# Optimization experiments

Measured on AMD Instinct MI355X. Metric: run time of the kernel, lower is better.

The kernel has to match this reference:

```python
import jax, jax.numpy as jnp
import numpy as np

B, T, C, H = 2, 2048, 2048, 16
HD = C // H  # 128
WINDOW = 2048


def setup_inputs() -> dict:
    key = jax.random.key(0)
    k0, k1, k2 = jax.random.split(key, 3)
    s = 0.02  # GPT-2 style init scale
    return {
        "x": jax.random.normal(k0, (B, T, C), jnp.float32),
        "w_attn": jax.random.normal(k1, (3 * C, C), jnp.float32) * s,
        "b_attn": jnp.zeros((3 * C,), jnp.float32),
        "w_proj": jax.random.normal(k2, (C, C), jnp.float32) * s,
        "b_proj": jnp.zeros((C,), jnp.float32),
    }


def reference(x, w_attn, b_attn, w_proj, b_proj):
    Bb, Tt, Cc = x.shape
    # fused qkv projection (torch Linear: y = x @ W^T + b)
    qkv = x @ w_attn.T + b_attn                       # [B, T, 3C]
    q, k, v = jnp.split(qkv, 3, axis=2)

    def to_heads(t):
        return t.reshape(Bb, Tt, H, HD).transpose(0, 2, 1, 3)  # [B, H, T, HD]

    q, k, v = to_heads(q), to_heads(k), to_heads(v)
    K = k.shape[2]  # kv length (== T, no past_kv)

    attn = jnp.einsum('bhqd,bhkd->bhqk', q, k) / jnp.sqrt(jnp.float32(HD))
    # Faithful to source: mask[:, :, T-1:T, :K] — single tril row T-1 broadcast
    # over all query positions (for prefill K==T this row is all ones).
    mask_row = jnp.arange(K) <= (Tt - 1)              # [K] bool
    attn = jnp.where(mask_row[None, None, None, :], attn, -jnp.inf)
    weights = jax.nn.softmax(attn, axis=-1)            # [B, H, T, K]
    # dropout p=0.0 (eval): identity
    ctx = jnp.einsum('bhqk,bhkd->bhqd', weights, v)    # [B, H, T, HD]
    ctx = ctx.transpose(0, 2, 1, 3).reshape(Bb, Tt, Cc)
    out = ctx @ w_proj.T + b_proj                      # [B, T, C]
    return (out, k, v)  # (context, present_kv)
```

## Files before the change

### kernel.cpp

```cpp
#include <hip/hip_runtime.h>
#include <hip/hip_bf16.h>
#include <cstdint>
#include <cstddef>
#include <cmath>

typedef __attribute__((ext_vector_type(8))) short short8;
typedef __attribute__((ext_vector_type(4))) short bf16x4;
typedef __attribute__((ext_vector_type(4))) float f32x4;

static constexpr int BB = 2, T = 2048, C = 2048, H = 16, HD = 128;
static constexpr int M = BB * T;
static constexpr size_t BTC = (size_t)BB * T * C;

__device__ __forceinline__ short f2bf(float f) {
    union { float f; uint32_t u; } v; v.f = f;
    uint32_t u = v.u;
    uint32_t r = (u + 0x7fffu + ((u >> 16) & 1u)) >> 16;
    return (short)r;
}

__device__ __forceinline__ short f2bf_fast(float f) {
    __hip_bfloat16 h = __float2bfloat16(f);
    return *reinterpret_cast<short*>(&h);
}

__device__ __forceinline__ void gl_lds16(const void* g, void* l) {
    __builtin_amdgcn_global_load_lds(
        (const __attribute__((address_space(1))) unsigned int*)g,
        (__attribute__((address_space(3))) unsigned int*)l, 16, 0, 0);
}

__global__ void cvt_bf16(const float* __restrict__ in, short* __restrict__ out, int n) {
    int i = (blockIdx.x * 256 + threadIdx.x) * 8;
    if (i >= n) return;
    float4 a = *(const float4*)(in + i);
    float4 b = *(const float4*)(in + i + 4);
    short8 o;
    o[0] = f2bf(a.x); o[1] = f2bf(a.y); o[2] = f2bf(a.z); o[3] = f2bf(a.w);
    o[4] = f2bf(b.x); o[5] = f2bf(b.y); o[6] = f2bf(b.z); o[7] = f2bf(b.w);
    *(short8*)(out + i) = o;
}

__launch_bounds__(512, 2)
__global__ void gemm_qkv256(const short* __restrict__ A, const short* __restrict__ Bw,
                            const float* __restrict__ bias, float* __restrict__ outF,
                            short* __restrict__ q_ws, short* __restrict__ k_ws) {
    extern __shared__ char lds[];
    constexpr int K = 2048, NKT = K / 64;
    constexpr int BUFSZ = 57344;

    int bid = blockIdx.x;
    int swz = (bid & 7) * 64 + (bid >> 3);
    int by = swz >> 5, bx = swz & 31;
    int row0 = by * 256, col0 = bx * 192;

    int t = threadIdx.x, w = t >> 6, l = t & 63;
    int lr = l & 15, lg = l >> 4;
    int wr = w >> 2, wc = w & 3;

    const char* Ab = (const char*)A;
    const char* Bb = (const char*)Bw;
    const char* srcb[7];
    int dstoff[7];
#pragma unroll
    for (int c = 0; c < 7; c++) {
        bool isA = c < 4;
        int coff = (isA ? c : c - 4) * 8192 + t * 16;
        int row = coff >> 7;
        int colb = (coff & 127) ^ ((row & 7) << 4);
        srcb[c] = isA ? Ab + (size_t)(row0 + row) * (K * 2) + colb
                      : Bb + (size_t)(col0 + row) * (K * 2) + colb;
        dstoff[c] = (isA ? 0 : 32768) + coff;
    }

    f32x4 acc[8][3] = {};

#pragma unroll
    for (int c = 0; c < 7; c++) gl_lds16(srcb[c], lds + dstoff[c]);
#pragma unroll
    for (int c = 0; c < 7; c++) gl_lds16(srcb[c] + 128, lds + BUFSZ + dstoff[c]);
    asm volatile("s_waitcnt vmcnt(7)" ::: "memory");
    __builtin_amdgcn_s_barrier();

    for (int kt = 0; kt < NKT; kt++) {
        const char* Abase = lds + (kt & 1) * BUFSZ;
        const char* Bbase = Abase + 32768;

        short8 bfr[3][2];
#pragma unroll
        for (int p = 0; p < 4; p++) {
            short8 af[2][2];
#pragma unroll
            for (int mi2 = 0; mi2 < 2; mi2++) {
                int row = wr * 128 + p * 32 + mi2 * 16 + lr;
#pragma unroll
                for (int ks = 0; ks < 2; ks++)
                    af[mi2][ks] = *(const short8*)(Abase + row * 128 +
                                  ((ks * 64 + lg * 16) ^ ((row & 7) << 4)));
            }
            if (p == 0) {
#pragma unroll
                for (int ni = 0; ni < 3; ni++) {
                    int row = wc * 48 + ni * 16 + lr;
#pragma unroll
                    for (int ks = 0; ks < 2; ks++)
                        bfr[ni][ks] = *(const short8*)(Bbase + row * 128 +
                                      ((ks * 64 + lg * 16) ^ ((row & 7) << 4)));
                }
            }
            __builtin_amdgcn_s_setprio(1);
#pragma unroll
            for (int ks = 0; ks < 2; ks++)
#pragma unroll
                for (int mi2 = 0; mi2 < 2; mi2++)
#pragma unroll
                    for (int ni = 0; ni < 3; ni++)
                        acc[p * 2 + mi2][ni] = __builtin_amdgcn_mfma_f32_16x16x32_bf16(
                            af[mi2][ks], bfr[ni][ks], acc[p * 2 + mi2][ni], 0, 0, 0);
            __builtin_amdgcn_s_setprio(0);
        }

        __builtin_amdgcn_s_barrier();
        if (kt + 2 < NKT) {
            int koff = (kt + 2) * 128;
            char* dbase = lds + (kt & 1) * BUFSZ;
#pragma unroll
            for (int c = 0; c < 7; c++) gl_lds16(srcb[c] + koff, dbase + dstoff[c]);
            asm volatile("s_waitcnt vmcnt(7)" ::: "memory");
        } else {
            asm volatile("s_waitcnt vmcnt(0)" ::: "memory");
        }
        __builtin_amdgcn_s_barrier();
    }

#pragma unroll
    for (int mi = 0; mi < 8; mi++) {
        int gr0 = row0 + wr * 128 + mi * 16 + lg * 4;
#pragma unroll
        for (int ni = 0; ni < 3; ni++) {
            int gc = col0 + wc * 48 + ni * 16 + lr;
            float bv = bias[gc];
            int sec = gc >> 11, cc = gc & 2047;
            int h = cc >> 7, d = cc & 127;
#pragma unroll
            for (int r = 0; r < 4; r++) {
                float val = acc[mi][ni][r] + bv;
                int gr = gr0 + r;
                int b = gr >> 11, tt = gr & 2047;
                size_t idx = ((size_t)(b * H + h) * T + tt) * HD + d;
                if (sec == 0) {
                    q_ws[idx] = f2bf(val);
                } else if (sec == 1) {
                    outF[BTC + idx] = val;
                    k_ws[idx] = f2bf(val);
                } else {
                    outF[2 * BTC + idx] = val;
                }
            }
        }
    }
}

__global__ void gemm_proj(const short* __restrict__ A, const short* __restrict__ Bw,
                          const float* __restrict__ bias, float* __restrict__ outF,
                          int Ndim, int K) {
    __shared__ __attribute__((aligned(16))) short As[128 * 32];
    __shared__ __attribute__((aligned(16))) short Bs[128 * 32];
    int t = threadIdx.x;
    int w = t >> 6, l = t & 63;
    int lr = l & 15, lg = l >> 4;
    int wr = w >> 1, wc = w & 1;
    int row0 = blockIdx.y * 128, col0 = blockIdx.x * 128;

    f32x4 acc[4][4] = {};

    for (int k0 = 0; k0 < K; k0 += 32) {
#pragma unroll
        for (int i = 0; i < 2; i++) {
            int off = i * 4096 + t * 16;
            int row = off >> 6;
            int cole = (off & 63) >> 1;
            gl_lds16(A + (size_t)(row0 + row) * K + k0 + cole, (char*)As + off);
            gl_lds16(Bw + (size_t)(col0 + row) * K + k0 + cole, (char*)Bs + off);
        }
        asm volatile("s_waitcnt vmcnt(0)" ::: "memory");
        __syncthreads();

        short8 af[4], bf[4];
#pragma unroll
        for (int mi = 0; mi < 4; mi++)
            af[mi] = *(const short8*)(As + (wr * 64 + mi * 16 + lr) * 32 + lg * 8);
#pragma unroll
        for (int ni = 0; ni < 4; ni++)
            bf[ni] = *(const short8*)(Bs + (wc * 64 + ni * 16 + lr) * 32 + lg * 8);
#pragma unroll
        for (int mi = 0; mi < 4; mi++)
#pragma unroll
            for (int ni = 0; ni < 4; ni++)
                acc[mi][ni] = __builtin_amdgcn_mfma_f32_16x16x32_bf16(af[mi], bf[ni], acc[mi][ni], 0, 0, 0);
        __syncthreads();
    }

#pragma unroll
    for (int mi = 0; mi < 4; mi++) {
        int gr0 = row0 + wr * 64 + mi * 16 + lg * 4;
#pragma unroll
        for (int ni = 0; ni < 4; ni++) {
            int gc = col0 + wc * 64 + ni * 16 + lr;
            float bv = bias[gc];
#pragma unroll
            for (int r = 0; r < 4; r++)
                outF[(size_t)(gr0 + r) * Ndim + gc] = acc[mi][ni][r] + bv;
        }
    }
}

__global__ void vtrans(const float* __restrict__ vin, short* __restrict__ vT) {
    __shared__ float tile[64 * 65];
    int blk = blockIdx.x;
    int bh = blk >> 6, rem = blk & 63;
    int t0 = (rem >> 1) * 64, d0 = (rem & 1) * 64;
    const float* src = vin + (size_t)bh * T * HD;
    short* dst = vT + (size_t)bh * HD * T;
    int t = threadIdx.x;
#pragma unroll
    for (int i = 0; i < 16; i++) {
        int idx = i * 256 + t;
        int r = idx >> 6, c = idx & 63;
        tile[r * 65 + c] = src[(size_t)(t0 + r) * HD + d0 + c];
    }
    __syncthreads();
#pragma unroll
    for (int i = 0; i < 16; i++) {
        int idx = i * 256 + t;
        int rd = idx >> 6, cc = idx & 63;
        dst[(size_t)(d0 + rd) * T + t0 + cc] = f2bf(tile[cc * 65 + rd]);
    }
}

__launch_bounds__(256, 2)
__global__ void attn_fwd(const short* __restrict__ q_ws, const short* __restrict__ k_ws,
                         const short* __restrict__ vT_ws, short* __restrict__ ctx) {
    __shared__ __attribute__((aligned(16))) char K_lds[2][64 * 256];
    __shared__ __attribute__((aligned(16))) char VT_lds[2][128 * 128];
    __shared__ __attribute__((aligned(16))) char P_lds[4][16 * 128];

    int bid = blockIdx.x;
    int blk = (bid & 7) * 64 + (bid >> 3);
    int bh = blk >> 4;
    int q0 = (blk & 15) * 128;
    int b = bh >> 4, h = bh & 15;
    int t = threadIdx.x, w = t >> 6, l = t & 63;
    int lr = l & 15, lg = l >> 4;
    int sw = (lr & 7) << 4;

    short8 qf[2][4];
#pragma unroll
    for (int qt = 0; qt < 2; qt++) {
        const short* Qp = q_ws + ((size_t)bh * T + q0 + w * 32 + qt * 16 + lr) * HD;
#pragma unroll
        for (int c = 0; c < 4; c++) qf[qt][c] = *(const short8*)(Qp + c * 32 + lg * 8);
    }

    const char* Kp = (const char*)(k_ws + (size_t)bh * T * HD);
    const short* VTp = vT_ws + (size_t)bh * HD * T;
    char* Pc = P_lds[w];

    const float SC = 0.12753123813884803f;
    float m[2] = {-INFINITY, -INFINITY}, lsum[2] = {0.f, 0.f};
    f32x4 acc[2][8] = {};

    auto STAGE = [&](int kt, int bsel) {
#pragma unroll
        for (int i = 0; i < 4; i++) {
            int off = i * 4096 + t * 16;
            int swzK = off ^ (((off >> 8) & 7) << 4);
            gl_lds16(Kp + (size_t)kt * 16384 + swzK, K_lds[bsel] + off);
            int swzV = off ^ (((off >> 7) & 7) << 4);
            int row = swzV >> 7, cole = (swzV & 127) >> 1;
            gl_lds16(VTp + (size_t)row * T + kt * 64 + cole, VT_lds[bsel] + off);
        }
    };

    STAGE(0, 0);
    asm volatile("s_waitcnt vmcnt(0)" ::: "memory");
    __syncthreads();

    for (int kt = 0; kt < T / 64; kt++) {
        int cur = kt & 1;
        if (kt + 1 < T / 64) STAGE(kt + 1, cur ^ 1);
        const char* Kc = K_lds[cur];
        const char* Vc = VT_lds[cur];

        f32x4 sacc[2][4] = {};
#pragma unroll
        for (int kj = 0; kj < 4; kj++) {
            int rowb = (kj * 16 + lr) * 256;
#pragma unroll
            for (int c = 0; c < 4; c++) {
                short8 kf = *(const short8*)(Kc + ((rowb + c * 64 + lg * 16) ^ sw));
                sacc[0][kj] = __builtin_amdgcn_mfma_f32_16x16x32_bf16(kf, qf[0][c], sacc[0][kj], 0, 0, 0);
                sacc[1][kj] = __builtin_amdgcn_mfma_f32_16x16x32_bf16(kf, qf[1][c], sacc[1][kj], 0, 0, 0);
            }
        }

#pragma unroll
        for (int qt = 0; qt < 2; qt++) {
            float t0 = fmaxf(fmaxf(sacc[qt][0][0], sacc[qt][0][1]), fmaxf(sacc[qt][0][2], sacc[qt][0][3]));
            float t1 = fmaxf(fmaxf(sacc[qt][1][0], sacc[qt][1][1]), fmaxf(sacc[qt][1][2], sacc[qt][1][3]));
            float t2 = fmaxf(fmaxf(sacc[qt][2][0], sacc[qt][2][1]), fmaxf(sacc[qt][2][2], sacc[qt][2][3]));
            float t3 = fmaxf(fmaxf(sacc[qt][3][0], sacc[qt][3][1]), fmaxf(sacc[qt][3][2], sacc[qt][3][3]));
            float xm = fmaxf(fmaxf(t0, t1), fmaxf(t2, t3)) * SC;
            xm = fmaxf(xm, __shfl_xor(xm, 16));
            xm = fmaxf(xm, __shfl_xor(xm, 32));

            if (!__all(xm <= m[qt] + 8.0f)) {
                float mn = fmaxf(m[qt], xm);
                float al = __builtin_exp2f(m[qt] - mn);
                m[qt] = mn;
                lsum[qt] *= al;
                float ar[4];
#pragma unroll
                for (int r = 0; r < 4; r++) ar[r] = __shfl(al, lg * 4 + r);
#pragma unroll
                for (int nj = 0; nj < 8; nj++)
#pragma unroll
                    for (int r = 0; r < 4; r++) acc[qt][nj][r] *= ar[r];
            }

            float s0 = 0.f;
#pragma unroll
            for (int kj = 0; kj < 4; kj++) {
                bf16x4 pk;
#pragma unroll
                for (int r = 0; r < 4; r++) {
                    float pv = __builtin_exp2f(__builtin_fmaf(sacc[qt][kj][r], SC, -m[qt]));
                    s0 += pv;
                    pk[r] = f2bf_fast(pv);
                }
                *(bf16x4*)(Pc + ((lr * 128 + kj * 32 + lg * 8) ^ sw)) = pk;
            }
            s0 += __shfl_xor(s0, 16);
            s0 += __shfl_xor(s0, 32);
            lsum[qt] += s0;

            asm volatile("s_waitcnt lgkmcnt(0)" ::: "memory");

#pragma unroll
            for (int c2 = 0; c2 < 2; c2++) {
                short8 pf = *(const short8*)(Pc + ((lr * 128 + c2 * 64 + lg * 16) ^ sw));
#pragma unroll
                for (int nj = 0; nj < 8; nj++) {
                    short8 vf = *(const short8*)(Vc + (((nj * 16 + lr) * 128 + c2 * 64 + lg * 16) ^ sw));
                    acc[qt][nj] = __builtin_amdgcn_mfma_f32_16x16x32_bf16(pf, vf, acc[qt][nj], 0, 0, 0);
                }
            }
        }

        asm volatile("s_waitcnt vmcnt(0)" ::: "memory");
        __syncthreads();
    }

#pragma unroll
    for (int qt = 0; qt < 2; qt++)
#pragma unroll
        for (int r = 0; r < 4; r++) {
            float rs = __shfl(lsum[qt], lg * 4 + r);
            float inv = 1.0f / rs;
            int tq = q0 + w * 32 + qt * 16 + lg * 4 + r;
            size_t base = ((size_t)b * T + tq) * C + h * HD;
#pragma unroll
            for (int nj = 0; nj < 8; nj++)
                ctx[base + nj * 16 + lr] = f2bf_fast(acc[qt][nj][r] * inv);
        }
}

extern "C" void kernel_launch(void* const* d_in, const int* in_sizes, int n_in,
                              void* d_out, int out_size, void* d_ws, size_t ws_size,
                              hipStream_t stream) {
    const float* x      = (const float*)d_in[0];
    const float* w_attn = (const float*)d_in[1];
    const float* b_attn = (const float*)d_in[2];
    const float* w_proj = (const float*)d_in[3];
    const float* b_proj = (const float*)d_in[4];
    float* out = (float*)d_out;

    char* ws = (char*)d_ws;
    short* x_bf  = (short*)ws;
    short* wp_bf = (short*)ws;
    short* wa_bf = (short*)(ws + 16777216);
    short* ctx   = (short*)(ws + 16777216);
    short* vT    = (short*)(ws + 41943040);

    short* q_ws = (short*)d_out;
    short* k_ws = (short*)d_out + BTC;

    hipFuncSetAttribute((const void*)gemm_qkv256,
                        hipFuncAttributeMaxDynamicSharedMemorySize, 114688);

    cvt_bf16<<<4096, 256, 0, stream>>>(x, x_bf, (int)BTC);
    cvt_bf16<<<6144, 256, 0, stream>>>(w_attn, wa_bf, 3 * C * C);

    gemm_qkv256<<<512, 512, 114688, stream>>>(x_bf, wa_bf, b_attn, out, q_ws, k_ws);

    vtrans<<<2048, 256, 0, stream>>>(out + 2 * BTC, vT);
    cvt_bf16<<<2048, 256, 0, stream>>>(w_proj, wp_bf, C * C);

    attn_fwd<<<512, 256, 0, stream>>>(q_ws, k_ws, vT, ctx);

    gemm_proj<<<dim3(16, 32), 256, 0, stream>>>(ctx, wp_bf, b_proj, out, C, C);
}
```

Before: 303.2 us.

## Template 8-wave GEMM, interleave prefetch across phases, reuse for projection

Turns the QKV GEMM into a template parameterised by N-tile width and epilogue. The next tile's global-to-LDS prefetch is now spread across the four compute phases with barriers between them, instead of being issued all at once after compute. The output projection now uses this double-buffered 256x128 kernel in place of the simple single-buffered 128x128 GEMM. The extra per-phase barriers add sync cost, and the projection launches only 256 workgroups, which may leave some CUs idle.

```diff
diff --git a/kernel.cpp b/kernel.cpp
--- a/kernel.cpp
+++ b/kernel.cpp
@@ -41,52 +41,55 @@
     *(short8*)(out + i) = o;
 }
 
+template<int NI, int EPI, int NBX>
 __launch_bounds__(512, 2)
-__global__ void gemm_qkv256(const short* __restrict__ A, const short* __restrict__ Bw,
-                            const float* __restrict__ bias, float* __restrict__ outF,
-                            short* __restrict__ q_ws, short* __restrict__ k_ws) {
+__global__ void gemm8p(const short* __restrict__ A, const short* __restrict__ Bw,
+                       const float* __restrict__ bias, float* __restrict__ outF,
+                       short* __restrict__ q_ws, short* __restrict__ k_ws, int Ndim) {
     extern __shared__ char lds[];
     constexpr int K = 2048, NKT = K / 64;
-    constexpr int BUFSZ = 57344;
+    constexpr int NCH = 4 + NI;
+    constexpr int BUFSZ = 32768 + NI * 8192;
 
     int bid = blockIdx.x;
-    int swz = (bid & 7) * 64 + (bid >> 3);
-    int by = swz >> 5, bx = swz & 31;
-    int row0 = by * 256, col0 = bx * 192;
+    int nwg = gridDim.x;
+    int swz = (bid & 7) * (nwg >> 3) + (bid >> 3);
+    int by = swz / NBX, bx = swz % NBX;
+    int row0 = by * 256, col0 = bx * (NI * 64);
 
     int t = threadIdx.x, w = t >> 6, l = t & 63;
     int lr = l & 15, lg = l >> 4;
     int wr = w >> 2, wc = w & 3;
 
-    const char* Ab = (const char*)A;
-    const char* Bb = (const char*)Bw;
-    const char* srcb[7];
-    int dstoff[7];
-#pragma unroll
-    for (int c = 0; c < 7; c++) {
+    const char* srcb[NCH];
+    int dstoff[NCH];
+#pragma unroll
+    for (int c = 0; c < NCH; c++) {
         bool isA = c < 4;
         int coff = (isA ? c : c - 4) * 8192 + t * 16;
         int row = coff >> 7;
         int colb = (coff & 127) ^ ((row & 7) << 4);
-        srcb[c] = isA ? Ab + (size_t)(row0 + row) * (K * 2) + colb
-                      : Bb + (size_t)(col0 + row) * (K * 2) + colb;
+        srcb[c] = isA ? (const char*)A + (size_t)(row0 + row) * (K * 2) + colb
+                      : (const char*)Bw + (size_t)(col0 + row) * (K * 2) + colb;
         dstoff[c] = (isA ? 0 : 32768) + coff;
     }
 
-    f32x4 acc[8][3] = {};
-
-#pragma unroll
-    for (int c = 0; c < 7; c++) gl_lds16(srcb[c], lds + dstoff[c]);
-#pragma unroll
-    for (int c = 0; c < 7; c++) gl_lds16(srcb[c] + 128, lds + BUFSZ + dstoff[c]);
-    asm volatile("s_waitcnt vmcnt(7)" ::: "memory");
+    f32x4 acc[8][NI] = {};
+
+#pragma unroll
+    for (int c = 0; c < NCH; c++) gl_lds16(srcb[c], lds + dstoff[c]);
+#pragma unroll
+    for (int c = 0; c < NCH; c++) gl_lds16(srcb[c] + 128, lds + BUFSZ + dstoff[c]);
+    asm volatile("s_waitcnt vmcnt(%0)" :: "n"(NCH) : "memory");
     __builtin_amdgcn_s_barrier();
 
     for (int kt = 0; kt < NKT; kt++) {
-        const char* Abase = lds + (kt & 1) * BUFSZ;
-        const char* Bbase = Abase + 32768;
-
-        short8 bfr[3][2];
+        char* base = lds + (kt & 1) * BUFSZ;
+        const char* Bbase = base + 32768;
+        int koff = (kt + 2) * 128;
+        bool pf = (kt + 2 < NKT);
+
+        short8 bfr[NI][2];
 #pragma unroll
         for (int p = 0; p < 4; p++) {
             short8 af[2][2];
@@ -95,122 +98,87 @@
                 int row = wr * 128 + p * 32 + mi2 * 16 + lr;
 #pragma unroll
                 for (int ks = 0; ks < 2; ks++)
-                    af[mi2][ks] = *(const short8*)(Abase + row * 128 +
+                    af[mi2][ks] = *(const short8*)(base + row * 128 +
                                   ((ks * 64 + lg * 16) ^ ((row & 7) << 4)));
             }
             if (p == 0) {
 #pragma unroll
-                for (int ni = 0; ni < 3; ni++) {
-                    int row = wc * 48 + ni * 16 + lr;
+                for (int ni = 0; ni < NI; ni++) {
+                    int row = wc * (NI * 16) + ni * 16 + lr;
 #pragma unroll
                     for (int ks = 0; ks < 2; ks++)
                         bfr[ni][ks] = *(const short8*)(Bbase + row * 128 +
                                       ((ks * 64 + lg * 16) ^ ((row & 7) << 4)));
                 }
             }
+            __builtin_amdgcn_s_barrier();
             __builtin_amdgcn_s_setprio(1);
 #pragma unroll
             for (int ks = 0; ks < 2; ks++)
 #pragma unroll
                 for (int mi2 = 0; mi2 < 2; mi2++)
 #pragma unroll
-                    for (int ni = 0; ni < 3; ni++)
+                    for (int ni = 0; ni < NI; ni++)
                         acc[p * 2 + mi2][ni] = __builtin_amdgcn_mfma_f32_16x16x32_bf16(
                             af[mi2][ks], bfr[ni][ks], acc[p * 2 + mi2][ni], 0, 0, 0);
             __builtin_amdgcn_s_setprio(0);
-        }
-
-        __builtin_amdgcn_s_barrier();
-        if (kt + 2 < NKT) {
-            int koff = (kt + 2) * 128;
-            char* dbase = lds + (kt & 1) * BUFSZ;
-#pragma unroll
-            for (int c = 0; c < 7; c++) gl_lds16(srcb[c] + koff, dbase + dstoff[c]);
-            asm volatile("s_waitcnt vmcnt(7)" ::: "memory");
-        } else {
-            asm volatile("s_waitcnt vmcnt(0)" ::: "memory");
-        }
-        __builtin_amdgcn_s_barrier();
+            __builtin_amdgcn_sched_barrier(0);
+            __builtin_amdgcn_s_barrier();
+
+            if (p == 0 && pf) {
+                asm volatile("" ::: "memory");
+#pragma unroll
+                for (int c = 4; c < NCH; c++) gl_lds16(srcb[c] + koff, base + dstoff[c]);
+            }
+            if (p == 1 && pf) {
+                asm volatile("" ::: "memory");
+                gl_lds16(srcb[0] + koff, base + dstoff[0]);
+                gl_lds16(srcb[2] + koff, base + dstoff[2]);
+            }
+            if (p == 3) {
+                if (pf) {
+                    asm volatile("" ::: "memory");
+                    gl_lds16(srcb[1] + koff, base + dstoff[1]);
+                    gl_lds16(srcb[3] + koff, base + dstoff[3]);
+                    asm volatile("s_waitcnt vmcnt(%0)" :: "n"(NCH) : "memory");
+                } else {
+                    asm volatile("s_waitcnt vmcnt(0)" ::: "memory");
+                }
+                __builtin_amdgcn_s_barrier();
+            }
+        }
     }
 
 #pragma unroll
     for (int mi = 0; mi < 8; mi++) {
         int gr0 = row0 + wr * 128 + mi * 16 + lg * 4;
 #pragma unroll
-        for (int ni = 0; ni < 3; ni++) {
-            int gc = col0 + wc * 48 + ni * 16 + lr;
+        for (int ni = 0; ni < NI; ni++) {
+            int gc = col0 + wc * (NI * 16) + ni * 16 + lr;
             float bv = bias[gc];
-            int sec = gc >> 11, cc = gc & 2047;
-            int h = cc >> 7, d = cc & 127;
-#pragma unroll
-            for (int r = 0; r < 4; r++) {
-                float val = acc[mi][ni][r] + bv;
-                int gr = gr0 + r;
-                int b = gr >> 11, tt = gr & 2047;
-                size_t idx = ((size_t)(b * H + h) * T + tt) * HD + d;
-                if (sec == 0) {
-                    q_ws[idx] = f2bf(val);
-                } else if (sec == 1) {
-                    outF[BTC + idx] = val;
-                    k_ws[idx] = f2bf(val);
-                } else {
-                    outF[2 * BTC + idx] = val;
-                }
-            }
-        }
-    }
-}
-
-__global__ void gemm_proj(const short* __restrict__ A, const short* __restrict__ Bw,
-                          const float* __restrict__ bias, float* __restrict__ outF,
-                          int Ndim, int K) {
-    __shared__ __attribute__((aligned(16))) short As[128 * 32];
-    __shared__ __attribute__((aligned(16))) short Bs[128 * 32];
-    int t = threadIdx.x;
-    int w = t >> 6, l = t & 63;
-    int lr = l & 15, lg = l >> 4;
-    int wr = w >> 1, wc = w & 1;
-    int row0 = blockIdx.y * 128, col0 = blockIdx.x * 128;
-
-    f32x4 acc[4][4] = {};
-
-    for (int k0 = 0; k0 < K; k0 += 32) {
-#pragma unroll
-        for (int i = 0; i < 2; i++) {
-            int off = i * 4096 + t * 16;
-            int row = off >> 6;
-            int cole = (off & 63) >> 1;
-            gl_lds16(A + (size_t)(row0 + row) * K + k0 + cole, (char*)As + off);
-            gl_lds16(Bw + (size_t)(col0 + row) * K + k0 + cole, (char*)Bs + off);
-        }
-        asm volatile("s_waitcnt vmcnt(0)" ::: "memory");
-        __syncthreads();
-
-        short8 af[4], bf[4];
-#pragma unroll
-        for (int mi = 0; mi < 4; mi++)
-            af[mi] = *(const short8*)(As + (wr * 64 + mi * 16 + lr) * 32 + lg * 8);
-#pragma unroll
-        for (int ni = 0; ni < 4; ni++)
-            bf[ni] = *(const short8*)(Bs + (wc * 64 + ni * 16 + lr) * 32 + lg * 8);
-#pragma unroll
-        for (int mi = 0; mi < 4; mi++)
-#pragma unroll
-            for (int ni = 0; ni < 4; ni++)
-                acc[mi][ni] = __builtin_amdgcn_mfma_f32_16x16x32_bf16(af[mi], bf[ni], acc[mi][ni], 0, 0, 0);
-        __syncthreads();
-    }
-
-#pragma unroll
-    for (int mi = 0; mi < 4; mi++) {
-        int gr0 = row0 + wr * 64 + mi * 16 + lg * 4;
-#pragma unroll
-        for (int ni = 0; ni < 4; ni++) {
-            int gc = col0 + wc * 64 + ni * 16 + lr;
-            float bv = bias[gc];
-#pragma unroll
-            for (int r = 0; r < 4; r++)
-                outF[(size_t)(gr0 + r) * Ndim + gc] = acc[mi][ni][r] + bv;
+            if (EPI == 0) {
+                int sec = gc >> 11, cc = gc & 2047;
+                int h = cc >> 7, d = cc & 127;
+#pragma unroll
+                for (int r = 0; r < 4; r++) {
+                    float val = acc[mi][ni][r] + bv;
+                    int gr = gr0 + r;
+                    int b = gr >> 11, tt = gr & 2047;
+                    size_t idx = ((size_t)(b * H + h) * T + tt) * HD + d;
+                    if (sec == 0) {
+                        q_ws[idx] = f2bf(val);
+                    } else if (sec == 1) {
+                        outF[BTC + idx] = val;
+                        k_ws[idx] = f2bf(val);
+                    } else {
+                        outF[2 * BTC + idx] = val;
+                    }
+                }
+            } else {
+#pragma unroll
+                for (int r = 0; r < 4; r++)
+                    outF[(size_t)(gr0 + r) * Ndim + gc] = acc[mi][ni][r] + bv;
+            }
         }
     }
 }
@@ -395,18 +363,20 @@
     short* q_ws = (short*)d_out;
     short* k_ws = (short*)d_out + BTC;
 
-    hipFuncSetAttribute((const void*)gemm_qkv256,
+    hipFuncSetAttribute((const void*)gemm8p<3, 0, 32>,
                         hipFuncAttributeMaxDynamicSharedMemorySize, 114688);
+    hipFuncSetAttribute((const void*)gemm8p<2, 1, 16>,
+                        hipFuncAttributeMaxDynamicSharedMemorySize, 98304);
 
     cvt_bf16<<<4096, 256, 0, stream>>>(x, x_bf, (int)BTC);
     cvt_bf16<<<6144, 256, 0, stream>>>(w_attn, wa_bf, 3 * C * C);
 
-    gemm_qkv256<<<512, 512, 114688, stream>>>(x_bf, wa_bf, b_attn, out, q_ws, k_ws);
+    gemm8p<3, 0, 32><<<512, 512, 114688, stream>>>(x_bf, wa_bf, b_attn, out, q_ws, k_ws, 6144);
 
     vtrans<<<2048, 256, 0, stream>>>(out + 2 * BTC, vT);
     cvt_bf16<<<2048, 256, 0, stream>>>(w_proj, wp_bf, C * C);
 
     attn_fwd<<<512, 256, 0, stream>>>(q_ws, k_ws, vT, ctx);
 
-    gemm_proj<<<dim3(16, 32), 256, 0, stream>>>(ctx, wp_bf, b_proj, out, C, C);
-}
+    gemm8p<2, 1, 16><<<256, 512, 98304, stream>>>(ctx, wp_bf, b_proj, out, nullptr, nullptr, 2048);
+}
```

Result: faster. 293.7 us (-3.1%).

## Fuse V transpose into QKV GEMM epilogue and pipeline projection GEMM

Applied to the files above, without the earlier changes.

The QKV GEMM epilogue now writes the bf16 transposed V directly, so the separate vtrans kernel and its re-read of fp32 V are gone. The output projection GEMM is rewritten with double-buffered LDS prefetch two k-steps ahead, XOR-swizzled LDS layout, a swizzled block order and s_setprio around the MFMAs. It also raises occupancy via launch bounds. The fused transpose writes are strided (stride T) from the GEMM epilogue, which could cost more than the removed kernel.

```diff
diff --git a/kernel.cpp b/kernel.cpp
--- a/kernel.cpp
+++ b/kernel.cpp
@@ -44,7 +44,8 @@
 __launch_bounds__(512, 2)
 __global__ void gemm_qkv256(const short* __restrict__ A, const short* __restrict__ Bw,
                             const float* __restrict__ bias, float* __restrict__ outF,
-                            short* __restrict__ q_ws, short* __restrict__ k_ws) {
+                            short* __restrict__ q_ws, short* __restrict__ k_ws,
+                            short* __restrict__ vT) {
     extern __shared__ char lds[];
     constexpr int K = 2048, NKT = K / 64;
     constexpr int BUFSZ = 57344;
@@ -147,7 +148,8 @@
                 float val = acc[mi][ni][r] + bv;
                 int gr = gr0 + r;
                 int b = gr >> 11, tt = gr & 2047;
-                size_t idx = ((size_t)(b * H + h) * T + tt) * HD + d;
+                int bh = b * H + h;
+                size_t idx = ((size_t)bh * T + tt) * HD + d;
                 if (sec == 0) {
                     q_ws[idx] = f2bf(val);
                 } else if (sec == 1) {
@@ -155,50 +157,82 @@
                     k_ws[idx] = f2bf(val);
                 } else {
                     outF[2 * BTC + idx] = val;
+                    vT[((size_t)bh * HD + d) * T + tt] = f2bf(val);
                 }
             }
         }
     }
 }
 
-__global__ void gemm_proj(const short* __restrict__ A, const short* __restrict__ Bw,
-                          const float* __restrict__ bias, float* __restrict__ outF,
-                          int Ndim, int K) {
-    __shared__ __attribute__((aligned(16))) short As[128 * 32];
-    __shared__ __attribute__((aligned(16))) short Bs[128 * 32];
-    int t = threadIdx.x;
-    int w = t >> 6, l = t & 63;
+__launch_bounds__(256, 4)
+__global__ void gemm_proj32(const short* __restrict__ A, const short* __restrict__ Bw,
+                            const float* __restrict__ bias, float* __restrict__ outF) {
+    __shared__ __attribute__((aligned(16))) char lds[2][16384];
+    constexpr int K = 2048, NKT = K / 32;
+
+    int bid = blockIdx.x;
+    int swz = (bid & 7) * 64 + (bid >> 3);
+    int by = swz >> 4, bx = swz & 15;
+    int row0 = by * 128, col0 = bx * 128;
+
+    int t = threadIdx.x, w = t >> 6, l = t & 63;
     int lr = l & 15, lg = l >> 4;
     int wr = w >> 1, wc = w & 1;
-    int row0 = blockIdx.y * 128, col0 = blockIdx.x * 128;
+
+    const char* srcb[4];
+    int dstoff[4];
+#pragma unroll
+    for (int c = 0; c < 4; c++) {
+        bool isA = c < 2;
+        int coff = (isA ? c : c - 2) * 4096 + t * 16;
+        int row = coff >> 6;
+        int colb = (coff & 63) ^ (((row >> 1) & 3) << 4);
+        srcb[c] = isA ? (const char*)A + (size_t)(row0 + row) * (K * 2) + colb
+                      : (const char*)Bw + (size_t)(col0 + row) * (K * 2) + colb;
+        dstoff[c] = (isA ? 0 : 8192) + coff;
+    }
 
     f32x4 acc[4][4] = {};
 
-    for (int k0 = 0; k0 < K; k0 += 32) {
-#pragma unroll
-        for (int i = 0; i < 2; i++) {
-            int off = i * 4096 + t * 16;
-            int row = off >> 6;
-            int cole = (off & 63) >> 1;
-            gl_lds16(A + (size_t)(row0 + row) * K + k0 + cole, (char*)As + off);
-            gl_lds16(Bw + (size_t)(col0 + row) * K + k0 + cole, (char*)Bs + off);
-        }
-        asm volatile("s_waitcnt vmcnt(0)" ::: "memory");
-        __syncthreads();
-
-        short8 af[4], bf[4];
-#pragma unroll
-        for (int mi = 0; mi < 4; mi++)
-            af[mi] = *(const short8*)(As + (wr * 64 + mi * 16 + lr) * 32 + lg * 8);
-#pragma unroll
-        for (int ni = 0; ni < 4; ni++)
-            bf[ni] = *(const short8*)(Bs + (wc * 64 + ni * 16 + lr) * 32 + lg * 8);
-#pragma unroll
-        for (int mi = 0; mi < 4; mi++)
+#pragma unroll
+    for (int c = 0; c < 4; c++) gl_lds16(srcb[c], lds[0] + dstoff[c]);
+#pragma unroll
+    for (int c = 0; c < 4; c++) gl_lds16(srcb[c] + 64, lds[1] + dstoff[c]);
+    asm volatile("s_waitcnt vmcnt(4)" ::: "memory");
+    __builtin_amdgcn_s_barrier();
+
+    for (int kt = 0; kt < NKT; kt++) {
+        char* base = lds[kt & 1];
+
+        short8 bfr[4];
+#pragma unroll
+        for (int ni = 0; ni < 4; ni++) {
+            int row = wc * 64 + ni * 16 + lr;
+            bfr[ni] = *(const short8*)(base + 8192 + row * 64 +
+                      ((lg * 16) ^ (((row >> 1) & 3) << 4)));
+        }
+        __builtin_amdgcn_s_setprio(1);
+#pragma unroll
+        for (int mi = 0; mi < 4; mi++) {
+            int row = wr * 64 + mi * 16 + lr;
+            short8 af = *(const short8*)(base + row * 64 +
+                        ((lg * 16) ^ (((row >> 1) & 3) << 4)));
 #pragma unroll
             for (int ni = 0; ni < 4; ni++)
-                acc[mi][ni] = __builtin_amdgcn_mfma_f32_16x16x32_bf16(af[mi], bf[ni], acc[mi][ni], 0, 0, 0);
-        __syncthreads();
+                acc[mi][ni] = __builtin_amdgcn_mfma_f32_16x16x32_bf16(af, bfr[ni], acc[mi][ni], 0, 0, 0);
+        }
+        __builtin_amdgcn_s_setprio(0);
+
+        __builtin_amdgcn_s_barrier();
+        if (kt + 2 < NKT) {
+            int koff = (kt + 2) * 64;
+#pragma unroll
+            for (int c = 0; c < 4; c++) gl_lds16(srcb[c] + koff, base + dstoff[c]);
+            asm volatile("s_waitcnt vmcnt(4)" ::: "memory");
+        } else {
+            asm volatile("s_waitcnt vmcnt(0)" ::: "memory");
+        }
+        __builtin_amdgcn_s_barrier();
     }
 
 #pragma unroll
@@ -210,31 +244,8 @@
             float bv = bias[gc];
 #pragma unroll
             for (int r = 0; r < 4; r++)
-                outF[(size_t)(gr0 + r) * Ndim + gc] = acc[mi][ni][r] + bv;
-        }
-    }
-}
-
-__global__ void vtrans(const float* __restrict__ vin, short* __restrict__ vT) {
-    __shared__ float tile[64 * 65];
-    int blk = blockIdx.x;
-    int bh = blk >> 6, rem = blk & 63;
-    int t0 = (rem >> 1) * 64, d0 = (rem & 1) * 64;
-    const float* src = vin + (size_t)bh * T * HD;
-    short* dst = vT + (size_t)bh * HD * T;
-    int t = threadIdx.x;
-#pragma unroll
-    for (int i = 0; i < 16; i++) {
-        int idx = i * 256 + t;
-        int r = idx >> 6, c = idx & 63;
-        tile[r * 65 + c] = src[(size_t)(t0 + r) * HD + d0 + c];
-    }
-    __syncthreads();
-#pragma unroll
-    for (int i = 0; i < 16; i++) {
-        int idx = i * 256 + t;
-        int rd = idx >> 6, cc = idx & 63;
-        dst[(size_t)(d0 + rd) * T + t0 + cc] = f2bf(tile[cc * 65 + rd]);
+                outF[(size_t)(gr0 + r) * 2048 + gc] = acc[mi][ni][r] + bv;
+        }
     }
 }
 
@@ -348,11 +359,11 @@
 
 #pragma unroll
             for (int c2 = 0; c2 < 2; c2++) {
-                short8 pf = *(const short8*)(Pc + ((lr * 128 + c2 * 64 + lg * 16) ^ sw));
+                short8 pf2 = *(const short8*)(Pc + ((lr * 128 + c2 * 64 + lg * 16) ^ sw));
 #pragma unroll
                 for (int nj = 0; nj < 8; nj++) {
                     short8 vf = *(const short8*)(Vc + (((nj * 16 + lr) * 128 + c2 * 64 + lg * 16) ^ sw));
-                    acc[qt][nj] = __builtin_amdgcn_mfma_f32_16x16x32_bf16(pf, vf, acc[qt][nj], 0, 0, 0);
+                    acc[qt][nj] = __builtin_amdgcn_mfma_f32_16x16x32_bf16(pf2, vf, acc[qt][nj], 0, 0, 0);
                 }
             }
         }
@@ -401,12 +412,11 @@
     cvt_bf16<<<4096, 256, 0, stream>>>(x, x_bf, (int)BTC);
     cvt_bf16<<<6144, 256, 0, stream>>>(w_attn, wa_bf, 3 * C * C);
 
-    gemm_qkv256<<<512, 512, 114688, stream>>>(x_bf, wa_bf, b_attn, out, q_ws, k_ws);
-
-    vtrans<<<2048, 256, 0, stream>>>(out + 2 * BTC, vT);
+    gemm_qkv256<<<512, 512, 114688, stream>>>(x_bf, wa_bf, b_attn, out, q_ws, k_ws, vT);
+
     cvt_bf16<<<2048, 256, 0, stream>>>(w_proj, wp_bf, C * C);
 
     attn_fwd<<<512, 256, 0, stream>>>(q_ws, k_ws, vT, ctx);
 
-    gemm_proj<<<dim3(16, 32), 256, 0, stream>>>(ctx, wp_bf, b_proj, out, C, C);
-}
+    gemm_proj32<<<512, 256, 0, stream>>>(ctx, wp_bf, b_proj, out);
+}
```

Measured after the change: 310.5 us. 1.02x slower.
